# Performance work log

Hardware: AMD Instinct MI355X
Metric: run time of the kernel (lower is better)

## Reference

```python
import jax, jax.numpy as jnp
import numpy as np

B, H, W, C = 4, 128, 128, 256
HEADS, DHEAD = 8, 32


def conv2d(x, w, b=None, groups=1, pad=0):
    # x: [N,C,H,W], w: [O, C//groups, kh, kw]
    out = jax.lax.conv_general_dilated(
        x, w, window_strides=(1, 1), padding=[(pad, pad), (pad, pad)],
        dimension_numbers=("NCHW", "OIHW", "NCHW"), feature_group_count=groups)
    if b is not None:
        out = out + b[None, :, None, None]
    return out


def setup_inputs() -> dict:
    key = jax.random.key(0)
    ks = jax.random.split(key, 16)
    g = lambda i, shape, s=0.02: jax.random.normal(ks[i], shape, jnp.float32) * s
    return {
        "x": jax.random.normal(ks[0], (B, H, W, C), jnp.float32),
        "mask": jax.random.uniform(ks[1], (1, C, H, W), jnp.float32),
        "wq": g(2, (C, C)),
        "wk": g(3, (C, C)),
        "wv": g(4, (C, C)),
        "rescale": jnp.ones((HEADS, 1, 1), jnp.float32),
        "wproj": g(5, (C, C)),
        "bproj": jnp.zeros((C,), jnp.float32),
        "mg_w1": g(6, (C, C, 1, 1)),
        "mg_b1": jnp.zeros((C,), jnp.float32),
        "mg_w2": g(7, (C, C, 1, 1)),
        "mg_b2": jnp.zeros((C,), jnp.float32),
        "mg_dw": g(8, (C, 1, 5, 5)),
        "mg_db": jnp.zeros((C,), jnp.float32),
        "be_w1": g(9, (C, 1, 3, 3)),
        "be_w2": g(10, (C, 1, 3, 3)),
    }


def _l2norm(t, axis):
    n = jnp.sqrt(jnp.sum(t * t, axis=axis, keepdims=True))
    return t / jnp.maximum(n, 1e-12)


def reference(x, mask, wq, wk, wv, rescale, wproj, bproj,
              mg_w1, mg_b1, mg_w2, mg_b2, mg_dw, mg_db, be_w1, be_w2):
    b, h, w, c = x.shape
    heads = rescale.shape[0]
    d = c // heads
    n = h * w

    xf = x.reshape(b, n, c)
    q_inp = xf @ wq   # [b,n,c]
    k_inp = xf @ wk
    v_inp = xf @ wv

    # MaskGuidedMechanism (h==w so shift_back is identity)
    m = conv2d(mask, mg_w1, mg_b1)                                   # [1,c,h,w]
    attn_map = jax.nn.sigmoid(conv2d(conv2d(m, mg_w2, mg_b2), mg_dw, mg_db, groups=c, pad=2))
    m = m * attn_map + m
    mask_emb = jnp.transpose(m, (0, 2, 3, 1))                        # [1,h,w,c]
    ma = jnp.broadcast_to(mask_emb, (b, h, w, c)).reshape(b, n, c)

    split = lambda t: t.reshape(b, n, heads, d).transpose(0, 2, 1, 3)  # [b,heads,n,d]
    q, k, v, ma = map(split, (q_inp, k_inp, v_inp, ma))
    v = v * ma

    # channel attention: normalize over token dim n
    qn = _l2norm(q, axis=2)
    kn = _l2norm(k, axis=2)
    attn = jnp.einsum("bhni,bhnj->bhij", kn, qn)                     # [b,heads,d,d]
    attn = jax.nn.softmax(attn * rescale, axis=-1)
    out = jnp.einsum("bhij,bhnj->bhin", attn, v)                     # [b,heads,d,n]

    out = out.transpose(0, 3, 1, 2).reshape(b, n, heads * d)         # [b,n,c]
    out_c = (out @ wproj + bproj).reshape(b, h, w, c)

    # band_emb: depthwise3x3 -> GELU(exact) -> depthwise3x3 on v_inp image
    v_img = v_inp.reshape(b, h, w, c).transpose(0, 3, 1, 2)          # [b,c,h,w]
    y = conv2d(v_img, be_w1, groups=c, pad=1)
    y = jax.nn.gelu(y, approximate=False)
    y = conv2d(y, be_w2, groups=c, pad=1)
    out_p = y.transpose(0, 2, 3, 1)

    return out_c + out_p
```

## Files before the change

### kernel.cpp

```cpp
#include <hip/hip_runtime.h>
#include <stdint.h>

#define B 4
#define HW 128
#define C 256
#define NTOK 16384
#define MALL 65536
#define HEADS 8
#define DH 32

typedef float f32x4 __attribute__((ext_vector_type(4)));
typedef short s16x8 __attribute__((ext_vector_type(8)));
typedef short s16x4 __attribute__((ext_vector_type(4)));
typedef __bf16 bf16x8 __attribute__((ext_vector_type(8)));

__device__ __forceinline__ float bf2f(unsigned short u) {
  union { unsigned int i; float f; } x;
  x.i = ((unsigned int)u) << 16;
  return x.f;
}
__device__ __forceinline__ unsigned short f2bf(float f) {
  union { float f; unsigned int i; } x;
  x.f = f;
  unsigned int lsb = (x.i >> 16) & 1u;
  unsigned int r = x.i + 0x7fffu + lsb;
  return (unsigned short)(r >> 16);
}

__device__ __forceinline__ void gload_lds16(const void* g, void* l) {
  auto gp = reinterpret_cast<const __attribute__((address_space(1))) unsigned int*>(
      reinterpret_cast<uintptr_t>(g));
  auto lp = reinterpret_cast<__attribute__((address_space(3))) unsigned int*>(
      reinterpret_cast<uintptr_t>(l));
  __builtin_amdgcn_global_load_lds(gp, lp, 16, 0, 0);
}

#define CFENCE asm volatile("" ::: "memory")
#define RAWBAR()                      \
  do {                                \
    CFENCE;                           \
    __builtin_amdgcn_s_barrier();     \
    CFENCE;                           \
  } while (0)
#define LDSBAR()                                        \
  do {                                                  \
    asm volatile("s_waitcnt lgkmcnt(0)" ::: "memory");  \
    __builtin_amdgcn_s_barrier();                       \
    CFENCE;                                             \
  } while (0)

__global__ __launch_bounds__(256) void cast_x_kernel(const float* __restrict__ x,
                                                     unsigned short* __restrict__ xb) {
  const size_t stride = (size_t)gridDim.x * blockDim.x * 4;
  for (size_t i = ((size_t)blockIdx.x * blockDim.x + threadIdx.x) * 4; i < (size_t)MALL * C;
       i += stride) {
    const float4 v = *(const float4*)&x[i];
    s16x4 o;
    o[0] = (short)f2bf(v.x);
    o[1] = (short)f2bf(v.y);
    o[2] = (short)f2bf(v.z);
    o[3] = (short)f2bf(v.w);
    *(s16x4*)&xb[i] = o;
  }
}

__global__ __launch_bounds__(256) void prep_w_kernel(
    const float* __restrict__ wq, const float* __restrict__ wk, const float* __restrict__ wv,
    const float* __restrict__ wproj, const float* __restrict__ w1, const float* __restrict__ w2,
    unsigned short* __restrict__ wqkvT, unsigned short* __restrict__ wprojT,
    unsigned short* __restrict__ w1b, unsigned short* __restrict__ w2b) {
  const int idx = blockIdx.x * 256 + threadIdx.x;
  const int mat = blockIdx.y;
  const int n = idx >> 8, k = idx & 255;
  switch (mat) {
    case 0: wqkvT[idx] = f2bf(wq[k * 256 + n]); break;
    case 1: wqkvT[65536 + idx] = f2bf(wk[k * 256 + n]); break;
    case 2: wqkvT[131072 + idx] = f2bf(wv[k * 256 + n]); break;
    case 3: wprojT[idx] = f2bf(wproj[k * 256 + n]); break;
    case 4: w1b[idx] = f2bf(w1[idx]); break;
    case 5: w2b[idx] = f2bf(w2[idx]); break;
  }
}

__global__ __launch_bounds__(1024) void tmask_kernel(const float* __restrict__ mask,
                                                     unsigned short* __restrict__ mT) {
  __shared__ float tile[32][33];
  const int p0 = blockIdx.x * 32, c0 = blockIdx.y * 32;
  const int tx = threadIdx.x & 31, ty = threadIdx.x >> 5;
  tile[ty][tx] = mask[(size_t)(c0 + ty) * NTOK + p0 + tx];
  __syncthreads();
  mT[(size_t)(p0 + ty) * C + c0 + tx] = f2bf(tile[tx][ty]);
}

__global__ __launch_bounds__(512) void gemm_bt256_kernel(
    const unsigned short* __restrict__ A, const unsigned short* __restrict__ Bt,
    const int nbn, const int mode, unsigned short* __restrict__ ob0,
    unsigned short* __restrict__ ob1, unsigned short* __restrict__ ob2,
    const float* __restrict__ bias, float* __restrict__ of32,
    const unsigned short* __restrict__ y2) {
  __shared__ alignas(16) unsigned short smem[32768];
  unsigned short* lAb = smem;
  unsigned short* lBb = smem + 16384;
  const int nwg = gridDim.x;
  const int bid = blockIdx.x;
  const int qd = nwg >> 3, rr = nwg & 7;
  const int xcd = bid & 7, sidx = bid >> 3;
  const int swz = (xcd < rr ? xcd * (qd + 1) : rr * (qd + 1) + (xcd - rr) * qd) + sidx;
  const int m0 = (swz / nbn) * 256;
  const int n0 = (swz % nbn) * 256;
  if (mode == 2) Bt += (size_t)(m0 >> 14) * 65536;
  const int t = threadIdx.x;
  const int w = t >> 6, l = t & 63;
  const int wr = w >> 2, wc = w & 3;
  const int lr = l & 15, lg = l >> 4;

  const int srow = t >> 2;
  const int ssl = (t & 3) ^ ((t >> 3) & 3);

  auto stageA = [&](int kt) {
    unsigned short* d = lAb + (kt & 1) * 8192;
    const size_t kb = ((size_t)kt * 32 + ssl * 8) * 2;
    gload_lds16((const char*)A + ((size_t)(m0 + srow) * 256) * 2 + kb, (char*)d + t * 16);
    gload_lds16((const char*)A + ((size_t)(m0 + 128 + srow) * 256) * 2 + kb,
                (char*)d + 8192 + t * 16);
  };
  auto stageB = [&](int kt) {
    unsigned short* d = lBb + (kt & 1) * 8192;
    const size_t kb = ((size_t)kt * 32 + ssl * 8) * 2;
    gload_lds16((const char*)Bt + ((size_t)(n0 + srow) * 256) * 2 + kb, (char*)d + t * 16);
    gload_lds16((const char*)Bt + ((size_t)(n0 + 128 + srow) * 256) * 2 + kb,
                (char*)d + 8192 + t * 16);
  };

  f32x4 acc[8][4];
#pragma unroll
  for (int m = 0; m < 8; ++m)
#pragma unroll
    for (int j = 0; j < 4; ++j) acc[m][j] = f32x4{0.f, 0.f, 0.f, 0.f};

  const int asl = (lg ^ ((lr >> 1) & 3)) * 8;
  const int aoff = lr * 32 + asl;
  const int awb = wr * 4096;
  const int boff = (wc >> 1) * 4096 + ((wc & 1) * 64 + lr) * 32 + asl;

  stageA(0); stageB(0);
  asm volatile("s_waitcnt vmcnt(0)" ::: "memory");
  RAWBAR();

#pragma unroll
  for (int kt = 0; kt < 8; ++kt) {
    const unsigned short* bufA = lAb + (kt & 1) * 8192;
    const unsigned short* bufB = lBb + (kt & 1) * 8192;
    if (kt < 7) { stageA(kt + 1); stageB(kt + 1); }
    bf16x8 bfr[4], af[4], af2[4];
#pragma unroll
    for (int j = 0; j < 4; ++j) bfr[j] = *(const bf16x8*)&bufB[boff + j * 512];
#pragma unroll
    for (int m = 0; m < 4; ++m) af[m] = *(const bf16x8*)&bufA[awb + aoff + m * 512];
#pragma unroll
    for (int m = 0; m < 4; ++m) af2[m] = *(const bf16x8*)&bufA[awb + aoff + (m + 4) * 512];
    __builtin_amdgcn_s_setprio(1);
#pragma unroll
    for (int m = 0; m < 4; ++m)
#pragma unroll
      for (int j = 0; j < 4; ++j)
        acc[m][j] = __builtin_amdgcn_mfma_f32_16x16x32_bf16(af[m], bfr[j], acc[m][j], 0, 0, 0);
#pragma unroll
    for (int m = 0; m < 4; ++m)
#pragma unroll
      for (int j = 0; j < 4; ++j)
        acc[m + 4][j] =
            __builtin_amdgcn_mfma_f32_16x16x32_bf16(af2[m], bfr[j], acc[m + 4][j], 0, 0, 0);
    __builtin_amdgcn_s_setprio(0);
    if (kt < 7) asm volatile("s_waitcnt vmcnt(0)" ::: "memory");
    RAWBAR();
  }

  if (mode == 0) {
    unsigned short* dst = (n0 < 256) ? ob0 : (n0 < 512 ? ob1 : ob2);
    unsigned short* eph = smem;
#pragma unroll
    for (int c = 0; c < 4; ++c) {
      LDSBAR();
      if (wr == (c >> 1)) {
#pragma unroll
        for (int mm = 0; mm < 4; ++mm) {
          const int m = (c & 1) * 4 + mm;
          const int lrow = mm * 16 + lg * 4;
#pragma unroll
          for (int j = 0; j < 4; ++j) {
            const int col = wc * 64 + j * 16 + lr;
#pragma unroll
            for (int r = 0; r < 4; ++r) eph[(lrow + r) * 264 + col] = f2bf(acc[m][j][r]);
          }
        }
      }
      LDSBAR();
      const int col16 = t & 31;
#pragma unroll
      for (int c2 = 0; c2 < 4; ++c2) {
        const int lrow = c2 * 16 + (t >> 5);
        const int grow = m0 + c * 64 + lrow;
        const s16x8 v = *(const s16x8*)&eph[lrow * 264 + col16 * 8];
        *(s16x8*)&dst[(size_t)grow * C + col16 * 8] = v;
      }
    }
  } else {
    float* ephf = (float*)smem;
    const int colc = t & 63;
    const f32x4 bv = *(const f32x4*)&bias[colc * 4];
#pragma unroll
    for (int c = 0; c < 8; ++c) {
      LDSBAR();
      if (wr == (c >> 2)) {
#pragma unroll
        for (int mm = 0; mm < 2; ++mm) {
          const int m = (c & 3) * 2 + mm;
          const int lrow = mm * 16 + lg * 4;
#pragma unroll
          for (int j = 0; j < 4; ++j) {
            const int col = wc * 64 + j * 16 + lr;
#pragma unroll
            for (int r = 0; r < 4; ++r) ephf[(lrow + r) * 260 + col] = acc[m][j][r];
          }
        }
      }
      LDSBAR();
#pragma unroll
      for (int c2 = 0; c2 < 4; ++c2) {
        const int lrow = c2 * 8 + (t >> 6);
        const int grow = m0 + c * 32 + lrow;
        const f32x4 v = *(const f32x4*)&ephf[lrow * 260 + colc * 4];
        const s16x4 yv = *(const s16x4*)&y2[(size_t)grow * C + colc * 4];
        f32x4 o;
#pragma unroll
        for (int e = 0; e < 4; ++e) o[e] = v[e] + bv[e] + bf2f((unsigned short)yv[e]);
        *(f32x4*)&of32[(size_t)grow * C + colc * 4] = o;
      }
    }
  }
}

__global__ __launch_bounds__(256) void gemm_bt_kernel(
    const unsigned short* __restrict__ A, const unsigned short* __restrict__ Bt, const int K,
    const int nbn, const int mode, unsigned short* __restrict__ ob0,
    unsigned short* __restrict__ ob1, unsigned short* __restrict__ ob2,
    const float* __restrict__ bias, float* __restrict__ of32) {
  __shared__ unsigned short lA[2][128 * 64];
  __shared__ unsigned short lB[2][128 * 64];
  const int nwg = gridDim.x;
  const int bid = blockIdx.x;
  const int qd = nwg >> 3, rr = nwg & 7;
  const int xcd = bid & 7, sidx = bid >> 3;
  const int swz = (xcd < rr ? xcd * (qd + 1) : rr * (qd + 1) + (xcd - rr) * qd) + sidx;
  const int m0 = (swz / nbn) * 128;
  const int n0 = (swz % nbn) * 128;
  const int t = threadIdx.x;
  const int w = t >> 6, l = t & 63;
  const int wr = w >> 1, wc = w & 1;
  const int lr = l & 15, lg = l >> 4;

  const int strow = (l >> 3);
  const int scolb = (((l & 7) ^ strow) << 4);

  f32x4 acc[4][4];
#pragma unroll
  for (int i = 0; i < 4; ++i)
#pragma unroll
    for (int j = 0; j < 4; ++j) acc[i][j] = f32x4{0.f, 0.f, 0.f, 0.f};

  auto stage = [&](int buf, int k0) {
#pragma unroll
    for (int s = 0; s < 4; ++s) {
      const int seg = w * 4 + s;
      const int row = seg * 8 + strow;
      gload_lds16((const char*)A + ((size_t)(m0 + row) * K + k0) * 2 + scolb,
                  (char*)&lA[buf][0] + seg * 1024 + (l & 7) * 16);
      gload_lds16((const char*)Bt + ((size_t)(n0 + row) * K + k0) * 2 + scolb,
                  (char*)&lB[buf][0] + seg * 1024 + (l & 7) * 16);
    }
  };
  auto compute = [&](int buf) {
#pragma unroll
    for (int kk = 0; kk < 64; kk += 32) {
      bf16x8 af[4], bfr[4];
      const int sbase = (kk >> 3) + lg;
      const int p = (sbase ^ (lr & 7)) << 3;
#pragma unroll
      for (int i = 0; i < 4; ++i)
        af[i] = *(const bf16x8*)&lA[buf][(wr * 64 + i * 16 + lr) * 64 + p];
#pragma unroll
      for (int j = 0; j < 4; ++j)
        bfr[j] = *(const bf16x8*)&lB[buf][(wc * 64 + j * 16 + lr) * 64 + p];
#pragma unroll
      for (int i = 0; i < 4; ++i)
#pragma unroll
        for (int j = 0; j < 4; ++j)
          acc[i][j] = __builtin_amdgcn_mfma_f32_16x16x32_bf16(af[i], bfr[j], acc[i][j], 0, 0, 0);
    }
  };

  stage(0, 0);
  __syncthreads();
  int cur = 0;
  for (int k0 = 64; k0 < K; k0 += 64) {
    stage(cur ^ 1, k0);
    compute(cur);
    __syncthreads();
    cur ^= 1;
  }
  compute(cur);

#pragma unroll
  for (int i = 0; i < 4; ++i) {
    const int grow = m0 + wr * 64 + i * 16 + lg * 4;
#pragma unroll
    for (int j = 0; j < 4; ++j) {
      const int gcol = n0 + wc * 64 + j * 16 + lr;
#pragma unroll
      for (int r = 0; r < 4; ++r) {
        const float v = acc[i][j][r];
        const size_t row = (size_t)(grow + r);
        if (mode == 0) {
          unsigned short* dst = (gcol < 256) ? ob0 : (gcol < 512 ? ob1 : ob2);
          dst[row * C + (gcol & 255)] = f2bf(v);
        } else if (mode == 1) {
          ob0[row * C + gcol] = f2bf(v + bias[gcol]);
        } else {
          const size_t idx = row * C + gcol;
          of32[idx] += v + bias[gcol];
        }
      }
    }
  }
}

__global__ __launch_bounds__(256) void mask_dw5_kernel(
    const unsigned short* __restrict__ m2, const unsigned short* __restrict__ m1,
    const float* __restrict__ dw, const float* __restrict__ db,
    unsigned short* __restrict__ memb) {
  __shared__ float wlds[25 * 256];
  __shared__ float blds[256];
  const int t = threadIdx.x;
  const int y = blockIdx.y;
  const int x0 = blockIdx.x * 16 + (t >> 6) * 4;
  const int cg = (t & 63) * 4;
#pragma unroll
  for (int e = 0; e < 25; ++e) wlds[e * 256 + t] = dw[t * 25 + e];
  blds[t] = db[t];
  __syncthreads();

  const f32x4 bias = *(const f32x4*)&blds[cg];
  f32x4 acc[4];
#pragma unroll
  for (int xi = 0; xi < 4; ++xi) acc[xi] = bias;

#pragma unroll
  for (int dy = 0; dy < 5; ++dy) {
    const int yy = y + dy - 2;
    if (yy < 0 || yy >= HW) continue;
    f32x4 col[8];
#pragma unroll
    for (int j = 0; j < 8; ++j) {
      const int xx = x0 - 2 + j;
      if (xx >= 0 && xx < HW) {
        const s16x4 v = *(const s16x4*)&m2[((size_t)yy * HW + xx) * C + cg];
        col[j][0] = bf2f((unsigned short)v[0]);
        col[j][1] = bf2f((unsigned short)v[1]);
        col[j][2] = bf2f((unsigned short)v[2]);
        col[j][3] = bf2f((unsigned short)v[3]);
      } else {
        col[j] = f32x4{0.f, 0.f, 0.f, 0.f};
      }
    }
#pragma unroll
    for (int dx = 0; dx < 5; ++dx) {
      const f32x4 wv = *(const f32x4*)&wlds[(dy * 5 + dx) * 256 + cg];
#pragma unroll
      for (int xi = 0; xi < 4; ++xi) acc[xi] += wv * col[dx + xi];
    }
  }

#pragma unroll
  for (int xi = 0; xi < 4; ++xi) {
    const size_t oi = ((size_t)y * HW + x0 + xi) * C + cg;
    const s16x4 mv = *(const s16x4*)&m1[oi];
    s16x4 o;
#pragma unroll
    for (int ch = 0; ch < 4; ++ch) {
      const float a = 1.f / (1.f + __expf(-acc[xi][ch]));
      o[ch] = (short)f2bf(bf2f((unsigned short)mv[ch]) * (1.f + a));
    }
    *(s16x4*)&memb[oi] = o;
  }
}

__global__ __launch_bounds__(256) void gram_kernel(const unsigned short* __restrict__ qb,
                                                   const unsigned short* __restrict__ kb,
                                                   float* __restrict__ Gpart,
                                                   float* __restrict__ ssq,
                                                   float* __restrict__ ssk) {
  const int chunk = blockIdx.x;
  const int h = blockIdx.y;
  const int b = blockIdx.z;
  __shared__ float flk[128 * 32], flq[128 * 32];
  const int t = threadIdx.x;
  const int wv = t >> 6;
  const int i0 = (t & 7) * 4, j0 = ((t >> 3) & 7) * 4;
  const int lrow = t >> 2, lcb = (t & 3) * 8;
  float acc[4][4] = {};
  float sq[8] = {}, sk[8] = {};
  for (int sub = 0; sub < 8; ++sub) {
    const size_t nbase = (size_t)b * NTOK + chunk * 1024 + sub * 128;
    __syncthreads();
#pragma unroll
    for (int it = 0; it < 2; ++it) {
      const int row = it * 64 + lrow;
      const s16x8 kv8 = *(const s16x8*)&kb[(nbase + row) * C + h * 32 + lcb];
      const s16x8 qv8 = *(const s16x8*)&qb[(nbase + row) * C + h * 32 + lcb];
      f32x4 ka, kbb, qa, qbb;
#pragma unroll
      for (int e = 0; e < 4; ++e) {
        ka[e] = bf2f((unsigned short)kv8[e]);
        kbb[e] = bf2f((unsigned short)kv8[e + 4]);
        qa[e] = bf2f((unsigned short)qv8[e]);
        qbb[e] = bf2f((unsigned short)qv8[e + 4]);
      }
#pragma unroll
      for (int e = 0; e < 4; ++e) {
        sk[e] += ka[e] * ka[e];
        sk[e + 4] += kbb[e] * kbb[e];
        sq[e] += qa[e] * qa[e];
        sq[e + 4] += qbb[e] * qbb[e];
      }
      *(f32x4*)&flk[row * 32 + lcb] = ka;
      *(f32x4*)&flk[row * 32 + lcb + 4] = kbb;
      *(f32x4*)&flq[row * 32 + lcb] = qa;
      *(f32x4*)&flq[row * 32 + lcb + 4] = qbb;
    }
    __syncthreads();
    for (int n = wv; n < 128; n += 4) {
      const f32x4 kv = *(const f32x4*)&flk[n * 32 + i0];
      const f32x4 qv = *(const f32x4*)&flq[n * 32 + j0];
#pragma unroll
      for (int a = 0; a < 4; ++a)
#pragma unroll
        for (int bb = 0; bb < 4; ++bb) acc[a][bb] += kv[a] * qv[bb];
    }
  }
  const int pc = chunk * 4 + wv;
  float* dst = Gpart + (((size_t)pc * B + b) * HEADS + h) * 1024;
#pragma unroll
  for (int a = 0; a < 4; ++a)
#pragma unroll
    for (int bb = 0; bb < 4; ++bb) dst[(i0 + a) * 32 + (j0 + bb)] = acc[a][bb];
  __syncthreads();
#pragma unroll
  for (int e = 0; e < 8; ++e) {
    flq[t * 8 + e] = sq[e];
    flk[t * 8 + e] = sk[e];
  }
  __syncthreads();
  if (t < 32) {
    const int tm = t >> 3, e = t & 7;
    float s1 = 0.f, s2 = 0.f;
    for (int k2 = 0; k2 < 64; ++k2) {
      const int tt = tm + k2 * 4;
      s1 += flq[tt * 8 + e];
      s2 += flk[tt * 8 + e];
    }
    ssq[((size_t)b * 16 + chunk) * C + h * 32 + t] = s1;
    ssk[((size_t)b * 16 + chunk) * C + h * 32 + t] = s2;
  }
}

__global__ __launch_bounds__(256) void softmax_kernel(
    const float* __restrict__ Gpart, const float* __restrict__ ssq,
    const float* __restrict__ ssk, const float* __restrict__ rescale,
    unsigned short* __restrict__ attnb) {
  const int h = blockIdx.x, b = blockIdx.y;
  const int t = threadIdx.x;
  __shared__ float G[1024];
  __shared__ float nq[32], nk[32];
#pragma unroll
  for (int e = 0; e < 4; ++e) {
    const int cell = e * 256 + t;
    float s = 0.f;
    for (int pc = 0; pc < 64; ++pc)
      s += Gpart[(((size_t)pc * B + b) * HEADS + h) * 1024 + cell];
    G[cell] = s;
  }
  if (t < 64) {
    const int d = t & 31;
    const float* ss = (t < 32) ? ssq : ssk;
    float s = 0.f;
    for (int ch = 0; ch < 16; ++ch) s += ss[((size_t)b * 16 + ch) * C + h * 32 + d];
    const float nn = fmaxf(sqrtf(s), 1e-12f);
    if (t < 32) nq[d] = nn;
    else nk[d] = nn;
  }
  __syncthreads();
  if (t < 32) {
    const int i = t;
    const float rs = rescale[h];
    float row[32];
    float mx = -1e30f;
#pragma unroll
    for (int j = 0; j < 32; ++j) {
      const float v = G[i * 32 + j] / (nk[i] * nq[j]) * rs;
      row[j] = v;
      mx = fmaxf(mx, v);
    }
    float sum = 0.f;
#pragma unroll
    for (int j = 0; j < 32; ++j) {
      const float e = expf(row[j] - mx);
      row[j] = e;
      sum += e;
    }
    const float inv = 1.f / sum;
#pragma unroll
    for (int j = 0; j < 32; ++j)
      attnb[(((size_t)b * HEADS + h) * 32 + i) * 32 + j] = f2bf(row[j] * inv);
  }
}

__global__ __launch_bounds__(256) void weff_kernel(const unsigned short* __restrict__ attnb,
                                                   const unsigned short* __restrict__ wprojT,
                                                   unsigned short* __restrict__ weff) {
  const int b = blockIdx.y;
  const int co0 = blockIdx.x * 64;
  const int t = threadIdx.x;
  __shared__ float att[8192];
  for (int e = t; e < 8192; e += 256) att[e] = bf2f(attnb[(size_t)b * 8192 + e]);
  __syncthreads();
  const int o = co0 + (t & 63);
  const int hq = t >> 6;
#pragma unroll
  for (int hh = 0; hh < 2; ++hh) {
    const int h = hq * 2 + hh;
    float wp[32];
#pragma unroll
    for (int i = 0; i < 32; ++i) wp[i] = bf2f(wprojT[(size_t)o * 256 + h * 32 + i]);
    for (int j4 = 0; j4 < 8; ++j4) {
      f32x4 s = {0.f, 0.f, 0.f, 0.f};
#pragma unroll
      for (int i = 0; i < 32; ++i) {
        const f32x4 a4 = *(const f32x4*)&att[(h * 32 + i) * 32 + j4 * 4];
        s += wp[i] * a4;
      }
      s16x4 oo;
#pragma unroll
      for (int e = 0; e < 4; ++e) oo[e] = (short)f2bf(s[e]);
      *(s16x4*)&weff[((size_t)b * 256 + o) * 256 + h * 32 + j4 * 4] = oo;
    }
  }
}

__global__ __launch_bounds__(256) void vma_kernel(const unsigned short* __restrict__ vb,
                                                  const unsigned short* __restrict__ memb,
                                                  unsigned short* __restrict__ vma) {
  const size_t n8 = (size_t)MALL * C / 8;
  const size_t stride = (size_t)gridDim.x * blockDim.x;
  for (size_t i8 = (size_t)blockIdx.x * blockDim.x + threadIdx.x; i8 < n8; i8 += stride) {
    const s16x8 vv = *(const s16x8*)&vb[i8 * 8];
    const s16x8 mm = *(const s16x8*)&memb[(i8 & ((size_t)NTOK * C / 8 - 1)) * 8];
    s16x8 o;
#pragma unroll
    for (int e = 0; e < 8; ++e)
      o[e] = (short)f2bf(bf2f((unsigned short)vv[e]) * bf2f((unsigned short)mm[e]));
    *(s16x8*)&vma[i8 * 8] = o;
  }
}

__global__ __launch_bounds__(512) void dw3_kernel(const unsigned short* __restrict__ in,
                                                  const float* __restrict__ wgt,
                                                  unsigned short* __restrict__ out_bf,
                                                  float* __restrict__ out_f32,
                                                  const int do_gelu, const int write_f32) {
  const int y = blockIdx.x;
  const int b = blockIdx.y;
  const int t = threadIdx.x;
  const int cg = (t & 63) * 4;
  const int x0 = (t >> 6) * 16;
  float w[9][4];
#pragma unroll
  for (int e = 0; e < 9; ++e)
#pragma unroll
    for (int ch = 0; ch < 4; ++ch) w[e][ch] = wgt[(cg + ch) * 9 + e];
  const int ym = y - 1, yp = y + 1;
  const bool hm = (ym >= 0), hp = (yp < HW);
  const size_t base = (size_t)b * NTOK * C + cg;
  auto ld4 = [&](int yy, int xx) -> f32x4 {
    const s16x4 v = *(const s16x4*)&in[base + ((size_t)yy * HW + xx) * C];
    f32x4 f;
    f[0] = bf2f((unsigned short)v[0]);
    f[1] = bf2f((unsigned short)v[1]);
    f[2] = bf2f((unsigned short)v[2]);
    f[3] = bf2f((unsigned short)v[3]);
    return f;
  };
  const f32x4 zero = {0.f, 0.f, 0.f, 0.f};
  f32x4 a0, a1, a2, b0, b1, b2;
  if (x0 > 0) {
    a0 = hm ? ld4(ym, x0 - 1) : zero;
    a1 = ld4(y, x0 - 1);
    a2 = hp ? ld4(yp, x0 - 1) : zero;
  } else {
    a0 = a1 = a2 = zero;
  }
  b0 = hm ? ld4(ym, x0) : zero;
  b1 = ld4(y, x0);
  b2 = hp ? ld4(yp, x0) : zero;
  for (int xi = 0; xi < 16; ++xi) {
    const int x = x0 + xi;
    f32x4 c0, c1, c2;
    if (x + 1 < HW) {
      c0 = hm ? ld4(ym, x + 1) : zero;
      c1 = ld4(y, x + 1);
      c2 = hp ? ld4(yp, x + 1) : zero;
    } else {
      c0 = c1 = c2 = zero;
    }
    float res[4];
#pragma unroll
    for (int ch = 0; ch < 4; ++ch) {
      float r = w[0][ch] * a0[ch] + w[1][ch] * b0[ch] + w[2][ch] * c0[ch] +
                w[3][ch] * a1[ch] + w[4][ch] * b1[ch] + w[5][ch] * c1[ch] +
                w[6][ch] * a2[ch] + w[7][ch] * b2[ch] + w[8][ch] * c2[ch];
      if (do_gelu) r = 0.5f * r * (1.f + erff(r * 0.70710678118654752f));
      res[ch] = r;
    }
    const size_t oi = base + ((size_t)y * HW + x) * C;
    if (write_f32) {
      const f32x4 o = {res[0], res[1], res[2], res[3]};
      *(f32x4*)&out_f32[oi] = o;
    } else {
      s16x4 o;
      o[0] = (short)f2bf(res[0]);
      o[1] = (short)f2bf(res[1]);
      o[2] = (short)f2bf(res[2]);
      o[3] = (short)f2bf(res[3]);
      *(s16x4*)&out_bf[oi] = o;
    }
    a0 = b0; a1 = b1; a2 = b2;
    b0 = c0; b1 = c1; b2 = c2;
  }
}

extern "C" void kernel_launch(void* const* d_in, const int* in_sizes, int n_in, void* d_out,
                              int out_size, void* d_ws, size_t ws_size, hipStream_t stream) {
  (void)in_sizes; (void)n_in; (void)out_size; (void)ws_size;
  const float* x = (const float*)d_in[0];
  const float* maskp = (const float*)d_in[1];
  const float* wq = (const float*)d_in[2];
  const float* wk = (const float*)d_in[3];
  const float* wv = (const float*)d_in[4];
  const float* rescale = (const float*)d_in[5];
  const float* wproj = (const float*)d_in[6];
  const float* bproj = (const float*)d_in[7];
  const float* mg_w1 = (const float*)d_in[8];
  const float* mg_b1 = (const float*)d_in[9];
  const float* mg_w2 = (const float*)d_in[10];
  const float* mg_b2 = (const float*)d_in[11];
  const float* mg_dw = (const float*)d_in[12];
  const float* mg_db = (const float*)d_in[13];
  const float* be_w1 = (const float*)d_in[14];
  const float* be_w2 = (const float*)d_in[15];
  float* out = (float*)d_out;
  char* ws = (char*)d_ws;

  unsigned short* xb = (unsigned short*)(ws + 0ull);
  unsigned short* qb = (unsigned short*)(ws + 33554432ull);
  unsigned short* kb = (unsigned short*)(ws + 67108864ull);
  unsigned short* vb = (unsigned short*)(ws + 100663296ull);
  unsigned short* mT = (unsigned short*)(ws + 134217728ull);
  unsigned short* m1b = (unsigned short*)(ws + 142606336ull);
  unsigned short* m2b = (unsigned short*)(ws + 150994944ull);
  unsigned short* wqkvT = (unsigned short*)(ws + 159383552ull);
  unsigned short* wprojT = (unsigned short*)(ws + 159776768ull);
  unsigned short* w1b = (unsigned short*)(ws + 159907840ull);
  unsigned short* w2b = (unsigned short*)(ws + 160038912ull);
  float* ssq = (float*)(ws + 160169984ull);
  float* ssk = (float*)(ws + 160432128ull);
  unsigned short* attnb = (unsigned short*)(ws + 160694272ull);
  float* Gpart = (float*)m2b;
  unsigned short* memb = mT;
  unsigned short* vma = xb;
  unsigned short* y1 = qb;
  unsigned short* y2 = kb;
  unsigned short* weff = m1b;

  cast_x_kernel<<<2048, 256, 0, stream>>>(x, xb);
  prep_w_kernel<<<dim3(256, 6), 256, 0, stream>>>(wq, wk, wv, wproj, mg_w1, mg_w2, wqkvT,
                                                  wprojT, w1b, w2b);
  tmask_kernel<<<dim3(512, 8), 1024, 0, stream>>>(maskp, mT);
  gemm_bt_kernel<<<256, 256, 0, stream>>>(mT, w1b, 256, 2, 1, m1b, nullptr, nullptr, mg_b1,
                                          nullptr);
  gemm_bt_kernel<<<256, 256, 0, stream>>>(m1b, w2b, 256, 2, 1, m2b, nullptr, nullptr, mg_b2,
                                          nullptr);
  mask_dw5_kernel<<<dim3(8, 128), 256, 0, stream>>>(m2b, m1b, mg_dw, mg_db, memb);
  gemm_bt256_kernel<<<768, 512, 0, stream>>>(xb, wqkvT, 3, 0, qb, kb, vb, nullptr, nullptr,
                                             nullptr);
  gram_kernel<<<dim3(16, 8, 4), 256, 0, stream>>>(qb, kb, Gpart, ssq, ssk);
  softmax_kernel<<<dim3(8, 4), 256, 0, stream>>>(Gpart, ssq, ssk, rescale, attnb);
  weff_kernel<<<dim3(4, 4), 256, 0, stream>>>(attnb, wprojT, weff);
  vma_kernel<<<2048, 256, 0, stream>>>(vb, memb, vma);
  dw3_kernel<<<dim3(128, 4), 512, 0, stream>>>(vb, be_w1, y1, nullptr, 1, 0);
  dw3_kernel<<<dim3(128, 4), 512, 0, stream>>>(y1, be_w2, y2, nullptr, 0, 0);
  gemm_bt256_kernel<<<256, 512, 0, stream>>>(vma, weff, 1, 2, nullptr, nullptr, nullptr,
                                             bproj, out, y2);
}
```

Baseline: 305.8 us.

## Fuse x cast into QKV GEMM and v*mask into projection GEMM with 128 tiles

Removes the standalone fp32-to-bf16 cast kernel by having the QKV GEMM load fp32 x directly and convert into LDS. It also removes the vma elementwise kernel by multiplying v by the mask embedding inside the projection GEMM's A-tile load. Both GEMMs move from 256x256 tiles with 512 threads to 128x128 tiles with 256 threads and more workgroups. This saves two full-tensor round trips through HBM, at the cost of register-staged A loads instead of direct global-to-LDS copies and less data reuse per tile.

```diff
diff --git a/kernel.cpp b/kernel.cpp
--- a/kernel.cpp
+++ b/kernel.cpp
@@ -36,33 +36,12 @@
 }
 
 #define CFENCE asm volatile("" ::: "memory")
-#define RAWBAR()                      \
-  do {                                \
-    CFENCE;                           \
-    __builtin_amdgcn_s_barrier();     \
-    CFENCE;                           \
-  } while (0)
 #define LDSBAR()                                        \
   do {                                                  \
     asm volatile("s_waitcnt lgkmcnt(0)" ::: "memory");  \
     __builtin_amdgcn_s_barrier();                       \
     CFENCE;                                             \
   } while (0)
-
-__global__ __launch_bounds__(256) void cast_x_kernel(const float* __restrict__ x,
-                                                     unsigned short* __restrict__ xb) {
-  const size_t stride = (size_t)gridDim.x * blockDim.x * 4;
-  for (size_t i = ((size_t)blockIdx.x * blockDim.x + threadIdx.x) * 4; i < (size_t)MALL * C;
-       i += stride) {
-    const float4 v = *(const float4*)&x[i];
-    s16x4 o;
-    o[0] = (short)f2bf(v.x);
-    o[1] = (short)f2bf(v.y);
-    o[2] = (short)f2bf(v.z);
-    o[3] = (short)f2bf(v.w);
-    *(s16x4*)&xb[i] = o;
-  }
-}
 
 __global__ __launch_bounds__(256) void prep_w_kernel(
     const float* __restrict__ wq, const float* __restrict__ wk, const float* __restrict__ wv,
@@ -92,151 +71,255 @@
   mT[(size_t)(p0 + ty) * C + c0 + tx] = f2bf(tile[tx][ty]);
 }
 
-__global__ __launch_bounds__(512) void gemm_bt256_kernel(
-    const unsigned short* __restrict__ A, const unsigned short* __restrict__ Bt,
-    const int nbn, const int mode, unsigned short* __restrict__ ob0,
-    unsigned short* __restrict__ ob1, unsigned short* __restrict__ ob2,
-    const float* __restrict__ bias, float* __restrict__ of32,
-    const unsigned short* __restrict__ y2) {
-  __shared__ alignas(16) unsigned short smem[32768];
-  unsigned short* lAb = smem;
-  unsigned short* lBb = smem + 16384;
+__global__ __launch_bounds__(256) void gemm128_qkv_kernel(
+    const float* __restrict__ X, const unsigned short* __restrict__ Bt,
+    unsigned short* __restrict__ q, unsigned short* __restrict__ k,
+    unsigned short* __restrict__ v) {
+  __shared__ alignas(16) unsigned short smem[16384];
   const int nwg = gridDim.x;
   const int bid = blockIdx.x;
   const int qd = nwg >> 3, rr = nwg & 7;
   const int xcd = bid & 7, sidx = bid >> 3;
   const int swz = (xcd < rr ? xcd * (qd + 1) : rr * (qd + 1) + (xcd - rr) * qd) + sidx;
-  const int m0 = (swz / nbn) * 256;
-  const int n0 = (swz % nbn) * 256;
-  if (mode == 2) Bt += (size_t)(m0 >> 14) * 65536;
+  const int m0 = (swz / 6) * 128;
+  const int n0 = (swz % 6) * 128;
   const int t = threadIdx.x;
   const int w = t >> 6, l = t & 63;
-  const int wr = w >> 2, wc = w & 3;
+  const int wr = w >> 1, wc = w & 1;
   const int lr = l & 15, lg = l >> 4;
 
-  const int srow = t >> 2;
-  const int ssl = (t & 3) ^ ((t >> 3) & 3);
-
-  auto stageA = [&](int kt) {
-    unsigned short* d = lAb + (kt & 1) * 8192;
-    const size_t kb = ((size_t)kt * 32 + ssl * 8) * 2;
-    gload_lds16((const char*)A + ((size_t)(m0 + srow) * 256) * 2 + kb, (char*)d + t * 16);
-    gload_lds16((const char*)A + ((size_t)(m0 + 128 + srow) * 256) * 2 + kb,
-                (char*)d + 8192 + t * 16);
-  };
-  auto stageB = [&](int kt) {
-    unsigned short* d = lBb + (kt & 1) * 8192;
-    const size_t kb = ((size_t)kt * 32 + ssl * 8) * 2;
-    gload_lds16((const char*)Bt + ((size_t)(n0 + srow) * 256) * 2 + kb, (char*)d + t * 16);
-    gload_lds16((const char*)Bt + ((size_t)(n0 + 128 + srow) * 256) * 2 + kb,
-                (char*)d + 8192 + t * 16);
-  };
-
-  f32x4 acc[8][4];
-#pragma unroll
-  for (int m = 0; m < 8; ++m)
-#pragma unroll
-    for (int j = 0; j < 4; ++j) acc[m][j] = f32x4{0.f, 0.f, 0.f, 0.f};
-
-  const int asl = (lg ^ ((lr >> 1) & 3)) * 8;
-  const int aoff = lr * 32 + asl;
-  const int awb = wr * 4096;
-  const int boff = (wc >> 1) * 4096 + ((wc & 1) * 64 + lr) * 32 + asl;
-
-  stageA(0); stageB(0);
+  const int r = t >> 1;
+  const int rm3 = r & 3;
+  const int p0s = (((t & 1) * 2 + 0) ^ rm3);
+  const int p1s = (((t & 1) * 2 + 1) ^ rm3);
+  const int br = t >> 2;
+  const int bsl = (t & 3) ^ (br & 3);
+
+  f32x4 va0, va1, va2, va3;
+  auto ALOAD = [&](int kt) {
+    const float* src = X + (size_t)(m0 + r) * 256 + kt * 32;
+    va0 = *(const f32x4*)(src + p0s * 8);
+    va1 = *(const f32x4*)(src + p0s * 8 + 4);
+    va2 = *(const f32x4*)(src + p1s * 8);
+    va3 = *(const f32x4*)(src + p1s * 8 + 4);
+  };
+  auto AWRITE = [&](int buf) {
+    s16x8 o0, o1;
+#pragma unroll
+    for (int e = 0; e < 4; ++e) {
+      o0[e] = (short)f2bf(va0[e]);
+      o0[e + 4] = (short)f2bf(va1[e]);
+      o1[e] = (short)f2bf(va2[e]);
+      o1[e + 4] = (short)f2bf(va3[e]);
+    }
+    unsigned short* d = smem + buf * 4096 + t * 16;
+    *(s16x8*)d = o0;
+    *(s16x8*)(d + 8) = o1;
+  };
+  auto STAGEB = [&](int kt, int buf) {
+    char* dbase = (char*)(smem + 8192 + buf * 4096);
+    gload_lds16(Bt + (size_t)(n0 + br) * 256 + kt * 32 + bsl * 8, dbase + t * 16);
+    gload_lds16(Bt + (size_t)(n0 + 64 + br) * 256 + kt * 32 + bsl * 8,
+                dbase + 4096 + t * 16);
+  };
+
+  f32x4 acc[4][4];
+#pragma unroll
+  for (int i = 0; i < 4; ++i)
+#pragma unroll
+    for (int j = 0; j < 4; ++j) acc[i][j] = f32x4{0.f, 0.f, 0.f, 0.f};
+
+  const int fsl = (lg ^ (lr & 3)) * 8;
+
+  ALOAD(0);
+  STAGEB(0, 0);
   asm volatile("s_waitcnt vmcnt(0)" ::: "memory");
-  RAWBAR();
+  AWRITE(0);
+  LDSBAR();
 
 #pragma unroll
   for (int kt = 0; kt < 8; ++kt) {
-    const unsigned short* bufA = lAb + (kt & 1) * 8192;
-    const unsigned short* bufB = lBb + (kt & 1) * 8192;
-    if (kt < 7) { stageA(kt + 1); stageB(kt + 1); }
-    bf16x8 bfr[4], af[4], af2[4];
-#pragma unroll
-    for (int j = 0; j < 4; ++j) bfr[j] = *(const bf16x8*)&bufB[boff + j * 512];
-#pragma unroll
-    for (int m = 0; m < 4; ++m) af[m] = *(const bf16x8*)&bufA[awb + aoff + m * 512];
-#pragma unroll
-    for (int m = 0; m < 4; ++m) af2[m] = *(const bf16x8*)&bufA[awb + aoff + (m + 4) * 512];
+    const int cur = kt & 1;
+    if (kt < 7) {
+      ALOAD(kt + 1);
+      STAGEB(kt + 1, cur ^ 1);
+    }
+    bf16x8 af[4], bfv[4];
+#pragma unroll
+    for (int j = 0; j < 4; ++j)
+      bfv[j] = *(const bf16x8*)&smem[8192 + cur * 4096 + (wc * 64 + j * 16 + lr) * 32 + fsl];
+#pragma unroll
+    for (int i = 0; i < 4; ++i)
+      af[i] = *(const bf16x8*)&smem[cur * 4096 + (wr * 64 + i * 16 + lr) * 32 + fsl];
     __builtin_amdgcn_s_setprio(1);
 #pragma unroll
-    for (int m = 0; m < 4; ++m)
+    for (int i = 0; i < 4; ++i)
 #pragma unroll
       for (int j = 0; j < 4; ++j)
-        acc[m][j] = __builtin_amdgcn_mfma_f32_16x16x32_bf16(af[m], bfr[j], acc[m][j], 0, 0, 0);
-#pragma unroll
-    for (int m = 0; m < 4; ++m)
-#pragma unroll
-      for (int j = 0; j < 4; ++j)
-        acc[m + 4][j] =
-            __builtin_amdgcn_mfma_f32_16x16x32_bf16(af2[m], bfr[j], acc[m + 4][j], 0, 0, 0);
+        acc[i][j] = __builtin_amdgcn_mfma_f32_16x16x32_bf16(af[i], bfv[j], acc[i][j], 0, 0, 0);
     __builtin_amdgcn_s_setprio(0);
-    if (kt < 7) asm volatile("s_waitcnt vmcnt(0)" ::: "memory");
-    RAWBAR();
-  }
-
-  if (mode == 0) {
-    unsigned short* dst = (n0 < 256) ? ob0 : (n0 < 512 ? ob1 : ob2);
-    unsigned short* eph = smem;
-#pragma unroll
-    for (int c = 0; c < 4; ++c) {
-      LDSBAR();
-      if (wr == (c >> 1)) {
-#pragma unroll
-        for (int mm = 0; mm < 4; ++mm) {
-          const int m = (c & 1) * 4 + mm;
-          const int lrow = mm * 16 + lg * 4;
-#pragma unroll
-          for (int j = 0; j < 4; ++j) {
-            const int col = wc * 64 + j * 16 + lr;
-#pragma unroll
-            for (int r = 0; r < 4; ++r) eph[(lrow + r) * 264 + col] = f2bf(acc[m][j][r]);
-          }
+    if (kt < 7) {
+      asm volatile("s_waitcnt vmcnt(0)" ::: "memory");
+      AWRITE(cur ^ 1);
+    }
+    LDSBAR();
+  }
+
+  unsigned short* dstp = (n0 < 256) ? q : (n0 < 512 ? k : v);
+  const int cbase = n0 & 255;
+  unsigned short* eph = smem;
+#pragma unroll
+  for (int c = 0; c < 2; ++c) {
+    if (c) LDSBAR();
+    if (wr == c) {
+#pragma unroll
+      for (int i = 0; i < 4; ++i) {
+        const int lbase = i * 16 + lg * 4;
+#pragma unroll
+        for (int j = 0; j < 4; ++j) {
+          const int col = wc * 64 + j * 16 + lr;
+#pragma unroll
+          for (int r2 = 0; r2 < 4; ++r2) eph[(lbase + r2) * 136 + col] = f2bf(acc[i][j][r2]);
         }
       }
-      LDSBAR();
-      const int col16 = t & 31;
-#pragma unroll
-      for (int c2 = 0; c2 < 4; ++c2) {
-        const int lrow = c2 * 16 + (t >> 5);
-        const int grow = m0 + c * 64 + lrow;
-        const s16x8 v = *(const s16x8*)&eph[lrow * 264 + col16 * 8];
-        *(s16x8*)&dst[(size_t)grow * C + col16 * 8] = v;
-      }
-    }
-  } else {
-    float* ephf = (float*)smem;
-    const int colc = t & 63;
-    const f32x4 bv = *(const f32x4*)&bias[colc * 4];
-#pragma unroll
-    for (int c = 0; c < 8; ++c) {
-      LDSBAR();
-      if (wr == (c >> 2)) {
-#pragma unroll
-        for (int mm = 0; mm < 2; ++mm) {
-          const int m = (c & 3) * 2 + mm;
-          const int lrow = mm * 16 + lg * 4;
-#pragma unroll
-          for (int j = 0; j < 4; ++j) {
-            const int col = wc * 64 + j * 16 + lr;
-#pragma unroll
-            for (int r = 0; r < 4; ++r) ephf[(lrow + r) * 260 + col] = acc[m][j][r];
-          }
+    }
+    LDSBAR();
+#pragma unroll
+    for (int c2 = 0; c2 < 4; ++c2) {
+      const int lrow = c2 * 16 + (t >> 4);
+      const s16x8 vv = *(const s16x8*)&eph[lrow * 136 + (t & 15) * 8];
+      *(s16x8*)&dstp[(size_t)(m0 + c * 64 + lrow) * C + cbase + (t & 15) * 8] = vv;
+    }
+  }
+}
+
+__global__ __launch_bounds__(256) void gemm128_proj_kernel(
+    const unsigned short* __restrict__ V, const unsigned short* __restrict__ memb,
+    const unsigned short* __restrict__ weff, const float* __restrict__ bias,
+    const unsigned short* __restrict__ y2, float* __restrict__ out) {
+  __shared__ alignas(16) unsigned short smem[16384];
+  const int nwg = gridDim.x;
+  const int bid = blockIdx.x;
+  const int qd = nwg >> 3, rr = nwg & 7;
+  const int xcd = bid & 7, sidx = bid >> 3;
+  const int swz = (xcd < rr ? xcd * (qd + 1) : rr * (qd + 1) + (xcd - rr) * qd) + sidx;
+  const int m0 = (swz >> 1) * 128;
+  const int n0 = (swz & 1) * 128;
+  const unsigned short* Bt = weff + (size_t)(m0 >> 14) * 65536;
+  const int t = threadIdx.x;
+  const int w = t >> 6, l = t & 63;
+  const int wr = w >> 1, wc = w & 1;
+  const int lr = l & 15, lg = l >> 4;
+
+  const int r = t >> 1;
+  const int rm3 = r & 3;
+  const int p0s = (((t & 1) * 2 + 0) ^ rm3);
+  const int p1s = (((t & 1) * 2 + 1) ^ rm3);
+  const size_t mrow = (size_t)((m0 & 16383) + r);
+  const int br = t >> 2;
+  const int bsl = (t & 3) ^ (br & 3);
+
+  s16x8 va0, va1, ma0, ma1;
+  auto ALOAD = [&](int kt) {
+    const unsigned short* vsrc = V + (size_t)(m0 + r) * 256 + kt * 32;
+    const unsigned short* msrc = memb + mrow * 256 + kt * 32;
+    va0 = *(const s16x8*)(vsrc + p0s * 8);
+    ma0 = *(const s16x8*)(msrc + p0s * 8);
+    va1 = *(const s16x8*)(vsrc + p1s * 8);
+    ma1 = *(const s16x8*)(msrc + p1s * 8);
+  };
+  auto AWRITE = [&](int buf) {
+    s16x8 o0, o1;
+#pragma unroll
+    for (int e = 0; e < 8; ++e) {
+      o0[e] = (short)f2bf(bf2f((unsigned short)va0[e]) * bf2f((unsigned short)ma0[e]));
+      o1[e] = (short)f2bf(bf2f((unsigned short)va1[e]) * bf2f((unsigned short)ma1[e]));
+    }
+    unsigned short* d = smem + buf * 4096 + t * 16;
+    *(s16x8*)d = o0;
+    *(s16x8*)(d + 8) = o1;
+  };
+  auto STAGEB = [&](int kt, int buf) {
+    char* dbase = (char*)(smem + 8192 + buf * 4096);
+    gload_lds16(Bt + (size_t)(n0 + br) * 256 + kt * 32 + bsl * 8, dbase + t * 16);
+    gload_lds16(Bt + (size_t)(n0 + 64 + br) * 256 + kt * 32 + bsl * 8,
+                dbase + 4096 + t * 16);
+  };
+
+  f32x4 acc[4][4];
+#pragma unroll
+  for (int i = 0; i < 4; ++i)
+#pragma unroll
+    for (int j = 0; j < 4; ++j) acc[i][j] = f32x4{0.f, 0.f, 0.f, 0.f};
+
+  const int fsl = (lg ^ (lr & 3)) * 8;
+
+  ALOAD(0);
+  STAGEB(0, 0);
+  asm volatile("s_waitcnt vmcnt(0)" ::: "memory");
+  AWRITE(0);
+  LDSBAR();
+
+#pragma unroll
+  for (int kt = 0; kt < 8; ++kt) {
+    const int cur = kt & 1;
+    if (kt < 7) {
+      ALOAD(kt + 1);
+      STAGEB(kt + 1, cur ^ 1);
+    }
+    bf16x8 af[4], bfv[4];
+#pragma unroll
+    for (int j = 0; j < 4; ++j)
+      bfv[j] = *(const bf16x8*)&smem[8192 + cur * 4096 + (wc * 64 + j * 16 + lr) * 32 + fsl];
+#pragma unroll
+    for (int i = 0; i < 4; ++i)
+      af[i] = *(const bf16x8*)&smem[cur * 4096 + (wr * 64 + i * 16 + lr) * 32 + fsl];
+    __builtin_amdgcn_s_setprio(1);
+#pragma unroll
+    for (int i = 0; i < 4; ++i)
+#pragma unroll
+      for (int j = 0; j < 4; ++j)
+        acc[i][j] = __builtin_amdgcn_mfma_f32_16x16x32_bf16(af[i], bfv[j], acc[i][j], 0, 0, 0);
+    __builtin_amdgcn_s_setprio(0);
+    if (kt < 7) {
+      asm volatile("s_waitcnt vmcnt(0)" ::: "memory");
+      AWRITE(cur ^ 1);
+    }
+    LDSBAR();
+  }
+
+  float* ephf = (float*)smem;
+  const int colc = t & 31;
+  const int trow = t >> 5;
+  const int gc4 = n0 + colc * 4;
+  const f32x4 bv = *(const f32x4*)&bias[gc4];
+#pragma unroll
+  for (int c = 0; c < 4; ++c) {
+    if (c) LDSBAR();
+    if (wr == (c >> 1)) {
+#pragma unroll
+      for (int b2 = 0; b2 < 2; ++b2) {
+        const int ii = (c & 1) * 2 + b2;
+        const int lbase = b2 * 16 + lg * 4;
+#pragma unroll
+        for (int j = 0; j < 4; ++j) {
+          const int col = wc * 64 + j * 16 + lr;
+#pragma unroll
+          for (int r2 = 0; r2 < 4; ++r2) ephf[(lbase + r2) * 132 + col] = acc[ii][j][r2];
         }
       }
-      LDSBAR();
-#pragma unroll
-      for (int c2 = 0; c2 < 4; ++c2) {
-        const int lrow = c2 * 8 + (t >> 6);
-        const int grow = m0 + c * 32 + lrow;
-        const f32x4 v = *(const f32x4*)&ephf[lrow * 260 + colc * 4];
-        const s16x4 yv = *(const s16x4*)&y2[(size_t)grow * C + colc * 4];
-        f32x4 o;
-#pragma unroll
-        for (int e = 0; e < 4; ++e) o[e] = v[e] + bv[e] + bf2f((unsigned short)yv[e]);
-        *(f32x4*)&of32[(size_t)grow * C + colc * 4] = o;
-      }
+    }
+    LDSBAR();
+#pragma unroll
+    for (int c2 = 0; c2 < 4; ++c2) {
+      const int lrow = c2 * 8 + trow;
+      const int grow = m0 + c * 32 + lrow;
+      const f32x4 vv = *(const f32x4*)&ephf[lrow * 132 + colc * 4];
+      const s16x4 yv = *(const s16x4*)&y2[(size_t)grow * C + gc4];
+      f32x4 o;
+#pragma unroll
+      for (int e = 0; e < 4; ++e) o[e] = vv[e] + bv[e] + bf2f((unsigned short)yv[e]);
+      *(f32x4*)&out[(size_t)grow * C + gc4] = o;
     }
   }
 }
@@ -557,27 +640,10 @@
   }
 }
 
-__global__ __launch_bounds__(256) void vma_kernel(const unsigned short* __restrict__ vb,
-                                                  const unsigned short* __restrict__ memb,
-                                                  unsigned short* __restrict__ vma) {
-  const size_t n8 = (size_t)MALL * C / 8;
-  const size_t stride = (size_t)gridDim.x * blockDim.x;
-  for (size_t i8 = (size_t)blockIdx.x * blockDim.x + threadIdx.x; i8 < n8; i8 += stride) {
-    const s16x8 vv = *(const s16x8*)&vb[i8 * 8];
-    const s16x8 mm = *(const s16x8*)&memb[(i8 & ((size_t)NTOK * C / 8 - 1)) * 8];
-    s16x8 o;
-#pragma unroll
-    for (int e = 0; e < 8; ++e)
-      o[e] = (short)f2bf(bf2f((unsigned short)vv[e]) * bf2f((unsigned short)mm[e]));
-    *(s16x8*)&vma[i8 * 8] = o;
-  }
-}
-
 __global__ __launch_bounds__(512) void dw3_kernel(const unsigned short* __restrict__ in,
                                                   const float* __restrict__ wgt,
                                                   unsigned short* __restrict__ out_bf,
-                                                  float* __restrict__ out_f32,
-                                                  const int do_gelu, const int write_f32) {
+                                                  const int do_gelu) {
   const int y = blockIdx.x;
   const int b = blockIdx.y;
   const int t = threadIdx.x;
@@ -632,17 +698,12 @@
       res[ch] = r;
     }
     const size_t oi = base + ((size_t)y * HW + x) * C;
-    if (write_f32) {
-      const f32x4 o = {res[0], res[1], res[2], res[3]};
-      *(f32x4*)&out_f32[oi] = o;
-    } else {
-      s16x4 o;
-      o[0] = (short)f2bf(res[0]);
-      o[1] = (short)f2bf(res[1]);
-      o[2] = (short)f2bf(res[2]);
-      o[3] = (short)f2bf(res[3]);
-      *(s16x4*)&out_bf[oi] = o;
-    }
+    s16x4 o;
+    o[0] = (short)f2bf(res[0]);
+    o[1] = (short)f2bf(res[1]);
+    o[2] = (short)f2bf(res[2]);
+    o[3] = (short)f2bf(res[3]);
+    *(s16x4*)&out_bf[oi] = o;
     a0 = b0; a1 = b1; a2 = b2;
     b0 = c0; b1 = c1; b2 = c2;
   }
@@ -670,7 +731,6 @@
   float* out = (float*)d_out;
   char* ws = (char*)d_ws;
 
-  unsigned short* xb = (unsigned short*)(ws + 0ull);
   unsigned short* qb = (unsigned short*)(ws + 33554432ull);
   unsigned short* kb = (unsigned short*)(ws + 67108864ull);
   unsigned short* vb = (unsigned short*)(ws + 100663296ull);
@@ -686,12 +746,10 @@
   unsigned short* attnb = (unsigned short*)(ws + 160694272ull);
   float* Gpart = (float*)m2b;
   unsigned short* memb = mT;
-  unsigned short* vma = xb;
   unsigned short* y1 = qb;
   unsigned short* y2 = kb;
   unsigned short* weff = m1b;
 
-  cast_x_kernel<<<2048, 256, 0, stream>>>(x, xb);
   prep_w_kernel<<<dim3(256, 6), 256, 0, stream>>>(wq, wk, wv, wproj, mg_w1, mg_w2, wqkvT,
                                                   wprojT, w1b, w2b);
   tmask_kernel<<<dim3(512, 8), 1024, 0, stream>>>(maskp, mT);
@@ -700,14 +758,11 @@
   gemm_bt_kernel<<<256, 256, 0, stream>>>(m1b, w2b, 256, 2, 1, m2b, nullptr, nullptr, mg_b2,
                                           nullptr);
   mask_dw5_kernel<<<dim3(8, 128), 256, 0, stream>>>(m2b, m1b, mg_dw, mg_db, memb);
-  gemm_bt256_kernel<<<768, 512, 0, stream>>>(xb, wqkvT, 3, 0, qb, kb, vb, nullptr, nullptr,
-                                             nullptr);
+  gemm128_qkv_kernel<<<3072, 256, 0, stream>>>(x, wqkvT, qb, kb, vb);
   gram_kernel<<<dim3(16, 8, 4), 256, 0, stream>>>(qb, kb, Gpart, ssq, ssk);
   softmax_kernel<<<dim3(8, 4), 256, 0, stream>>>(Gpart, ssq, ssk, rescale, attnb);
   weff_kernel<<<dim3(4, 4), 256, 0, stream>>>(attnb, wprojT, weff);
-  vma_kernel<<<2048, 256, 0, stream>>>(vb, memb, vma);
-  dw3_kernel<<<dim3(128, 4), 512, 0, stream>>>(vb, be_w1, y1, nullptr, 1, 0);
-  dw3_kernel<<<dim3(128, 4), 512, 0, stream>>>(y1, be_w2, y2, nullptr, 0, 0);
-  gemm_bt256_kernel<<<256, 512, 0, stream>>>(vma, weff, 1, 2, nullptr, nullptr, nullptr,
-                                             bproj, out, y2);
-}
+  dw3_kernel<<<dim3(128, 4), 512, 0, stream>>>(vb, be_w1, y1, 1);
+  dw3_kernel<<<dim3(128, 4), 512, 0, stream>>>(y1, be_w2, y2, 0);
+  gemm128_proj_kernel<<<1024, 256, 0, stream>>>(vb, memb, weff, bproj, y2, out);
+}
```

After: 315.8 us. +3.3%, slower.
